# Kernel optimization log

Hardware: AMD Instinct MI355X
Metric: run time of the kernel (lower is better)

The kernel has to match this reference:

```python
import jax, jax.numpy as jnp
import numpy as np

N = 100000      # nodes
E = 1600000     # edges (before self loops)
F_IN = 256      # num_features
HID = 8         # hid per head, layer 1
H1 = 8          # in_head
H2 = 4          # out_head
NCLS = 40       # num_classes


def setup_inputs() -> dict:
    key = jax.random.key(0)
    ks = jax.random.split(key, 10)
    p = lambda k, shape: jax.random.normal(k, shape, jnp.float32) * 0.1
    d1 = H1 * HID   # 64
    d2 = H2 * NCLS  # 160
    return dict(
        x=jax.random.normal(ks[0], (N, F_IN), jnp.float32),
        edge_index=jax.random.randint(ks[1], (2, E), 0, N),
        Wl1=p(ks[2], (F_IN, d1)), bl1=jnp.zeros((d1,), jnp.float32),
        Wr1=p(ks[3], (F_IN, d1)), br1=jnp.zeros((d1,), jnp.float32),
        att1=p(ks[4], (H1, HID)), b1=jnp.zeros((d1,), jnp.float32),
        Wl2=p(ks[5], (d1, d2)), bl2=jnp.zeros((d2,), jnp.float32),
        Wr2=p(ks[6], (d1, d2)), br2=jnp.zeros((d2,), jnp.float32),
        att2=p(ks[7], (H2, NCLS)), b2=jnp.zeros((NCLS,), jnp.float32),
    )


def gatv2_conv(x, src, dst, Wl, bl, Wr, br, att, bias, heads, ch, concat):
    """PyG GATv2Conv (eval mode): lin_l -> source/messages, lin_r -> target."""
    n = x.shape[0]
    xl = (x @ Wl + bl).reshape(n, heads, ch)   # source-side features
    xr = (x @ Wr + br).reshape(n, heads, ch)   # target-side features
    # edge-wise attention logits: LeakyReLU(x_i + x_j) . att
    e = jax.nn.leaky_relu(xl[src] + xr[dst], 0.2)          # [E, H, C]
    logits = jnp.einsum('ehc,hc->eh', e, att)               # [E, H]
    # segment softmax over incoming edges of each destination node
    m = jax.ops.segment_max(logits, dst, num_segments=n)    # [N, H]
    ex = jnp.exp(logits - m[dst])
    s = jax.ops.segment_sum(ex, dst, num_segments=n)        # [N, H]
    alpha = ex / (s[dst] + 1e-16)                           # [E, H]
    # scatter-add weighted source messages
    out = jax.ops.segment_sum(xl[src] * alpha[:, :, None], dst, num_segments=n)  # [N, H, C]
    if concat:
        return out.reshape(n, heads * ch) + bias
    return out.mean(axis=1) + bias


def reference(x, edge_index, Wl1, bl1, Wr1, br1, att1, b1,
              Wl2, bl2, Wr2, br2, att2, b2):
    n = x.shape[0]
    loop = jnp.arange(n)
    # PyG GATv2Conv default add_self_loops=True
    src = jnp.concatenate([edge_index[0], loop])
    dst = jnp.concatenate([edge_index[1], loop])
    # eval mode: all dropout (input, inter-layer, attention) disabled
    h = gatv2_conv(x, src, dst, Wl1, bl1, Wr1, br1, att1, b1, H1, HID, True)
    h = jax.nn.elu(h)
    out = gatv2_conv(h, src, dst, Wl2, bl2, Wr2, br2, att2, b2, H2, NCLS, False)
    return jax.nn.log_softmax(out, axis=1)
```

## Files before the change

### kernel.cpp

```cpp
#include <hip/hip_runtime.h>
#include <math.h>

#define NN 100000
#define EE 1600000
#define FIN 256
#define D1 64
#define D2 160
#define C2 40
#define PK1 264
#define PK2 72
#define NBUCK 391
#define CAP 5000

typedef unsigned short u16;
typedef __attribute__((ext_vector_type(8))) short bf16x8;
typedef __attribute__((ext_vector_type(4))) float f32x4;

__device__ __forceinline__ float lrelu(float x){ return x > 0.f ? x : 0.2f*x; }
__device__ __forceinline__ float bf2f(u16 u){ return __uint_as_float((unsigned)u << 16); }
__device__ __forceinline__ u16 f2bf(float f){
  unsigned b = __float_as_uint(f);
  return (u16)((b + 0x7FFFu + ((b >> 16) & 1u)) >> 16);
}

__global__ __launch_bounds__(256) void part1_k(const int* __restrict__ ei,
                                               int* __restrict__ bcnt,
                                               int* __restrict__ csrtmp){
  __shared__ int hist[NBUCK];
  __shared__ int gbase[NBUCK];
  int t = threadIdx.x;
  for (int i = t; i < NBUCK; i += 256) hist[i] = 0;
  __syncthreads();
  int rb[8], rr[8], rv[8];
  #pragma unroll
  for (int q = 0; q < 8; ++q){
    int e = blockIdx.x*2048 + q*256 + t;
    rb[q] = -1;
    if (e < EE){
      int s = ei[e], d = ei[EE + e];
      int b = d >> 8;
      rb[q] = b;
      rv[q] = s | ((d & 255) << 17);
      rr[q] = atomicAdd(&hist[b], 1);
    }
  }
  __syncthreads();
  for (int i = t; i < NBUCK; i += 256)
    if (hist[i] > 0) gbase[i] = atomicAdd(&bcnt[i], hist[i]);
  __syncthreads();
  #pragma unroll
  for (int q = 0; q < 8; ++q){
    if (rb[q] >= 0){
      int pos = gbase[rb[q]] + rr[q];
      if (pos < CAP) csrtmp[rb[q]*CAP + pos] = rv[q];
    }
  }
}

__global__ __launch_bounds__(256) void sort_k(const int* __restrict__ bcnt,
                                              const int* __restrict__ csrtmp,
                                              int* __restrict__ csr,
                                              int* __restrict__ off,
                                              int* __restrict__ end){
  __shared__ int cnt[256];
  __shared__ int sc[256];
  __shared__ int cur[256];
  int b = blockIdx.x, t = threadIdx.x;
  int E = bcnt[b]; if (E > CAP) E = CAP;
  cnt[t] = 0;
  __syncthreads();
  for (int i = t; i < E; i += 256){
    int v = csrtmp[b*CAP + i];
    atomicAdd(&cnt[(v >> 17) & 255], 1);
  }
  __syncthreads();
  int x = cnt[t];
  sc[t] = x;
  __syncthreads();
  for (int o = 1; o < 256; o <<= 1){
    int v = (t >= o) ? sc[t - o] : 0;
    __syncthreads();
    sc[t] += v;
    __syncthreads();
  }
  int excl = sc[t] - x;
  cur[t] = excl;
  int n = (b << 8) + t;
  if (n < NN){
    off[n] = b*CAP + excl;
    end[n] = b*CAP + excl + x;
  }
  __syncthreads();
  for (int i = t; i < E; i += 256){
    int v = csrtmp[b*CAP + i];
    int p = atomicAdd(&cur[(v >> 17) & 255], 1);
    csr[b*CAP + p] = v & 0x1FFFF;
  }
}

__global__ __launch_bounds__(256) void gemm1_mfma(
    const float* __restrict__ X,
    const float* __restrict__ Wl, const float* __restrict__ bl,
    const float* __restrict__ Wr, const float* __restrict__ br,
    u16* __restrict__ outl, u16* __restrict__ outr){
  __shared__ u16 WB[128*PK1];
  int t = threadIdx.x;
  #pragma unroll
  for (int q = 0; q < 16; ++q){
    int idx = t + 256*q;
    int k = idx >> 4, c4 = idx & 15;
    float4 vl = *reinterpret_cast<const float4*>(Wl + (size_t)k*D1 + c4*4);
    float4 vr = *reinterpret_cast<const float4*>(Wr + (size_t)k*D1 + c4*4);
    WB[(c4*4+0)*PK1 + k] = f2bf(vl.x); WB[(c4*4+1)*PK1 + k] = f2bf(vl.y);
    WB[(c4*4+2)*PK1 + k] = f2bf(vl.z); WB[(c4*4+3)*PK1 + k] = f2bf(vl.w);
    WB[(64+c4*4+0)*PK1 + k] = f2bf(vr.x); WB[(64+c4*4+1)*PK1 + k] = f2bf(vr.y);
    WB[(64+c4*4+2)*PK1 + k] = f2bf(vr.z); WB[(64+c4*4+3)*PK1 + k] = f2bf(vr.w);
  }
  __syncthreads();
  int w = t >> 6, l = t & 63;
  int g = l >> 4;
  int arow = blockIdx.x*64 + w*16 + (l & 15);
  if (arow >= NN) arow = NN-1;
  const float* xp = X + (size_t)arow*FIN + g*8;
  f32x4 acc[8] = {};
  #pragma unroll
  for (int kk = 0; kk < 8; ++kk){
    float4 a0 = *reinterpret_cast<const float4*>(xp + kk*32);
    float4 a1 = *reinterpret_cast<const float4*>(xp + kk*32 + 4);
    union { bf16x8 v; u16 u[8]; } A;
    A.u[0]=f2bf(a0.x); A.u[1]=f2bf(a0.y); A.u[2]=f2bf(a0.z); A.u[3]=f2bf(a0.w);
    A.u[4]=f2bf(a1.x); A.u[5]=f2bf(a1.y); A.u[6]=f2bf(a1.z); A.u[7]=f2bf(a1.w);
    const u16* wb = WB + (l & 15)*PK1 + kk*32 + g*8;
    #pragma unroll
    for (int c = 0; c < 8; ++c){
      bf16x8 B = *reinterpret_cast<const bf16x8*>(wb + c*16*PK1);
      acc[c] = __builtin_amdgcn_mfma_f32_16x16x32_bf16(A.v, B, acc[c], 0, 0, 0);
    }
  }
  int ocol = l & 15;
  int orow0 = blockIdx.x*64 + w*16 + g*4;
  #pragma unroll
  for (int c = 0; c < 8; ++c){
    bool left = (c < 4);
    int col = (left ? c : c-4)*16 + ocol;
    u16* op = left ? outl : outr;
    float bv = (left ? bl : br)[col];
    #pragma unroll
    for (int r = 0; r < 4; ++r){
      int row = orow0 + r;
      if (row < NN) op[(size_t)row*D1 + col] = f2bf(acc[c][r] + bv);
    }
  }
}

__global__ __launch_bounds__(256) void gemm2_mfma(
    const u16* __restrict__ H,
    const float* __restrict__ Wl, const float* __restrict__ bl,
    const float* __restrict__ Wr, const float* __restrict__ br,
    u16* __restrict__ outl, u16* __restrict__ outr){
  __shared__ u16 WB[320*PK2];
  int t = threadIdx.x;
  #pragma unroll
  for (int q = 0; q < 10; ++q){
    int idx = t + 256*q;
    int k = idx / 40, c4 = idx % 40;
    float4 vl = *reinterpret_cast<const float4*>(Wl + (size_t)k*D2 + c4*4);
    float4 vr = *reinterpret_cast<const float4*>(Wr + (size_t)k*D2 + c4*4);
    WB[(c4*4+0)*PK2 + k] = f2bf(vl.x); WB[(c4*4+1)*PK2 + k] = f2bf(vl.y);
    WB[(c4*4+2)*PK2 + k] = f2bf(vl.z); WB[(c4*4+3)*PK2 + k] = f2bf(vl.w);
    WB[(160+c4*4+0)*PK2 + k] = f2bf(vr.x); WB[(160+c4*4+1)*PK2 + k] = f2bf(vr.y);
    WB[(160+c4*4+2)*PK2 + k] = f2bf(vr.z); WB[(160+c4*4+3)*PK2 + k] = f2bf(vr.w);
  }
  __syncthreads();
  int w = t >> 6, l = t & 63;
  int g = l >> 4;
  int arow = blockIdx.x*64 + w*16 + (l & 15);
  if (arow >= NN) arow = NN-1;
  const u16* hp = H + (size_t)arow*D1 + g*8;
  f32x4 acc[20] = {};
  #pragma unroll
  for (int kk = 0; kk < 2; ++kk){
    bf16x8 A = *reinterpret_cast<const bf16x8*>(hp + kk*32);
    const u16* wb = WB + (l & 15)*PK2 + kk*32 + g*8;
    #pragma unroll
    for (int c = 0; c < 20; ++c){
      bf16x8 B = *reinterpret_cast<const bf16x8*>(wb + c*16*PK2);
      acc[c] = __builtin_amdgcn_mfma_f32_16x16x32_bf16(A, B, acc[c], 0, 0, 0);
    }
  }
  int ocol = l & 15;
  int orow0 = blockIdx.x*64 + w*16 + g*4;
  #pragma unroll
  for (int c = 0; c < 20; ++c){
    bool left = (c < 10);
    int col = (left ? c : c-10)*16 + ocol;
    u16* op = left ? outl : outr;
    float bv = (left ? bl : br)[col];
    #pragma unroll
    for (int r = 0; r < 4; ++r){
      int row = orow0 + r;
      if (row < NN) op[(size_t)row*D2 + col] = f2bf(acc[c][r] + bv);
    }
  }
}

__global__ void l1_fused(const u16* __restrict__ xl, const u16* __restrict__ xr,
                         const int* __restrict__ off, const int* __restrict__ end,
                         const int* __restrict__ csr_src,
                         const float* __restrict__ att, const float* __restrict__ b,
                         u16* __restrict__ out){
  int n = blockIdx.x*4 + (threadIdx.x >> 6);
  if (n >= NN) return;
  int lane = threadIdx.x & 63;
  int g = lane >> 4, l = lane & 15;
  ushort4 xru = *reinterpret_cast<const ushort4*>(xr + (size_t)n*D1 + 4*l);
  float xrv[4] = {bf2f(xru.x), bf2f(xru.y), bf2f(xru.z), bf2f(xru.w)};
  float attv[4];
  #pragma unroll
  for (int k = 0; k < 4; ++k) attv[k] = att[4*l + k];
  ushort4 xsu = *reinterpret_cast<const ushort4*>(xl + (size_t)n*D1 + 4*l);
  float xsv[4] = {bf2f(xsu.x), bf2f(xsu.y), bf2f(xsu.z), bf2f(xsu.w)};
  float ts = 0.f;
  #pragma unroll
  for (int k = 0; k < 4; ++k) ts += lrelu(xsv[k] + xrv[k]) * attv[k];
  ts += __shfl_xor(ts, 1);
  float ps = (g == 0) ? __expf(ts) : 0.f;
  float s = ps, acc[4];
  #pragma unroll
  for (int k = 0; k < 4; ++k) acc[k] = ps * xsv[k];
  int e0 = off[n], e1 = end[n];
  int p = e0 + g;
  for (; p + 4 < e1; p += 8){
    int sa = csr_src[p], sb = csr_src[p+4];
    ushort4 ua = *reinterpret_cast<const ushort4*>(xl + (size_t)sa*D1 + 4*l);
    ushort4 ub = *reinterpret_cast<const ushort4*>(xl + (size_t)sb*D1 + 4*l);
    float xa[4] = {bf2f(ua.x), bf2f(ua.y), bf2f(ua.z), bf2f(ua.w)};
    float xb[4] = {bf2f(ub.x), bf2f(ub.y), bf2f(ub.z), bf2f(ub.w)};
    float ta = 0.f, tb = 0.f;
    #pragma unroll
    for (int k = 0; k < 4; ++k){
      ta += lrelu(xa[k] + xrv[k]) * attv[k];
      tb += lrelu(xb[k] + xrv[k]) * attv[k];
    }
    ta += __shfl_xor(ta, 1);
    tb += __shfl_xor(tb, 1);
    float pa = __expf(ta), pb = __expf(tb);
    s += pa + pb;
    #pragma unroll
    for (int k = 0; k < 4; ++k) acc[k] = fmaf(pa, xa[k], fmaf(pb, xb[k], acc[k]));
  }
  for (; p < e1; p += 4){
    int sa = csr_src[p];
    ushort4 ua = *reinterpret_cast<const ushort4*>(xl + (size_t)sa*D1 + 4*l);
    float xa[4] = {bf2f(ua.x), bf2f(ua.y), bf2f(ua.z), bf2f(ua.w)};
    float ta = 0.f;
    #pragma unroll
    for (int k = 0; k < 4; ++k) ta += lrelu(xa[k] + xrv[k]) * attv[k];
    ta += __shfl_xor(ta, 1);
    float pa = __expf(ta);
    s += pa;
    #pragma unroll
    for (int k = 0; k < 4; ++k) acc[k] = fmaf(pa, xa[k], acc[k]);
  }
  #pragma unroll
  for (int d = 16; d <= 32; d <<= 1){
    s += __shfl_xor(s, d);
    #pragma unroll
    for (int k = 0; k < 4; ++k) acc[k] += __shfl_xor(acc[k], d);
  }
  if (g == 0){
    float inv = 1.f / (s + 1e-16f);
    ushort4 o;
    float v0 = acc[0]*inv + b[4*l+0]; o.x = f2bf(v0 > 0.f ? v0 : expm1f(v0));
    float v1 = acc[1]*inv + b[4*l+1]; o.y = f2bf(v1 > 0.f ? v1 : expm1f(v1));
    float v2 = acc[2]*inv + b[4*l+2]; o.z = f2bf(v2 > 0.f ? v2 : expm1f(v2));
    float v3 = acc[3]*inv + b[4*l+3]; o.w = f2bf(v3 > 0.f ? v3 : expm1f(v3));
    *reinterpret_cast<ushort4*>(out + (size_t)n*D1 + 4*l) = o;
  }
}

__global__ void l2_fused(const u16* __restrict__ xl, const u16* __restrict__ xr,
                         const int* __restrict__ off, const int* __restrict__ end,
                         const int* __restrict__ csr_src,
                         const float* __restrict__ att, const float* __restrict__ b,
                         float* __restrict__ out){
  int n = blockIdx.x*4 + (threadIdx.x >> 6);
  if (n >= NN) return;
  int lane = threadIdx.x & 63;
  int g = lane >> 4, l = lane & 15;
  int c0 = 10*l;
  float xrv[10], attv[10];
  #pragma unroll
  for (int k2 = 0; k2 < 5; ++k2){
    ushort2 u = *reinterpret_cast<const ushort2*>(xr + (size_t)n*D2 + c0 + 2*k2);
    xrv[2*k2] = bf2f(u.x); xrv[2*k2+1] = bf2f(u.y);
  }
  #pragma unroll
  for (int k = 0; k < 10; ++k) attv[k] = att[c0 + k];
  float xsv[10];
  #pragma unroll
  for (int k2 = 0; k2 < 5; ++k2){
    ushort2 u = *reinterpret_cast<const ushort2*>(xl + (size_t)n*D2 + c0 + 2*k2);
    xsv[2*k2] = bf2f(u.x); xsv[2*k2+1] = bf2f(u.y);
  }
  float ts = 0.f;
  #pragma unroll
  for (int k = 0; k < 10; ++k) ts += lrelu(xsv[k] + xrv[k]) * attv[k];
  ts += __shfl_xor(ts, 1); ts += __shfl_xor(ts, 2);
  float ps = (g == 0) ? __expf(ts) : 0.f;
  float s = ps, acc[10];
  #pragma unroll
  for (int k = 0; k < 10; ++k) acc[k] = ps * xsv[k];
  int e0 = off[n], e1 = end[n];
  int p = e0 + g;
  for (; p + 4 < e1; p += 8){
    int sa = csr_src[p], sb = csr_src[p+4];
    float xa[10], xb[10];
    #pragma unroll
    for (int k2 = 0; k2 < 5; ++k2){
      ushort2 u = *reinterpret_cast<const ushort2*>(xl + (size_t)sa*D2 + c0 + 2*k2);
      xa[2*k2] = bf2f(u.x); xa[2*k2+1] = bf2f(u.y);
    }
    #pragma unroll
    for (int k2 = 0; k2 < 5; ++k2){
      ushort2 u = *reinterpret_cast<const ushort2*>(xl + (size_t)sb*D2 + c0 + 2*k2);
      xb[2*k2] = bf2f(u.x); xb[2*k2+1] = bf2f(u.y);
    }
    float ta = 0.f, tb = 0.f;
    #pragma unroll
    for (int k = 0; k < 10; ++k){
      ta += lrelu(xa[k] + xrv[k]) * attv[k];
      tb += lrelu(xb[k] + xrv[k]) * attv[k];
    }
    ta += __shfl_xor(ta, 1); ta += __shfl_xor(ta, 2);
    tb += __shfl_xor(tb, 1); tb += __shfl_xor(tb, 2);
    float pa = __expf(ta), pb = __expf(tb);
    s += pa + pb;
    #pragma unroll
    for (int k = 0; k < 10; ++k) acc[k] = fmaf(pa, xa[k], fmaf(pb, xb[k], acc[k]));
  }
  for (; p < e1; p += 4){
    int sa = csr_src[p];
    float xa[10];
    #pragma unroll
    for (int k2 = 0; k2 < 5; ++k2){
      ushort2 u = *reinterpret_cast<const ushort2*>(xl + (size_t)sa*D2 + c0 + 2*k2);
      xa[2*k2] = bf2f(u.x); xa[2*k2+1] = bf2f(u.y);
    }
    float ta = 0.f;
    #pragma unroll
    for (int k = 0; k < 10; ++k) ta += lrelu(xa[k] + xrv[k]) * attv[k];
    ta += __shfl_xor(ta, 1); ta += __shfl_xor(ta, 2);
    float pa = __expf(ta);
    s += pa;
    #pragma unroll
    for (int k = 0; k < 10; ++k) acc[k] = fmaf(pa, xa[k], acc[k]);
  }
  #pragma unroll
  for (int d = 16; d <= 32; d <<= 1){
    s += __shfl_xor(s, d);
    #pragma unroll
    for (int k = 0; k < 10; ++k) acc[k] += __shfl_xor(acc[k], d);
  }
  float inv = 1.f / (s + 1e-16f);
  float v[10];
  #pragma unroll
  for (int k = 0; k < 10; ++k){
    float o = acc[k] * inv;
    o += __shfl_xor(o, 4);
    o += __shfl_xor(o, 8);
    v[k] = o*0.25f + b[10*(l & 3) + k];
  }
  float mx = v[0];
  #pragma unroll
  for (int k = 1; k < 10; ++k) mx = fmaxf(mx, v[k]);
  mx = fmaxf(mx, __shfl_xor(mx, 1));
  mx = fmaxf(mx, __shfl_xor(mx, 2));
  float es = 0.f;
  #pragma unroll
  for (int k = 0; k < 10; ++k) es += __expf(v[k] - mx);
  es += __shfl_xor(es, 1);
  es += __shfl_xor(es, 2);
  float lse = mx + __logf(es);
  if (g == 0 && l < 4){
    float* op = out + (size_t)n*C2 + 10*l;
    #pragma unroll
    for (int k2 = 0; k2 < 5; ++k2)
      *reinterpret_cast<float2*>(op + 2*k2) = make_float2(v[2*k2] - lse, v[2*k2+1] - lse);
  }
}

extern "C" void kernel_launch(void* const* d_in, const int* in_sizes, int n_in,
                              void* d_out, int out_size, void* d_ws, size_t ws_size,
                              hipStream_t stream){
  const float* x    = (const float*)d_in[0];
  const int*   ei   = (const int*)  d_in[1];
  const float* Wl1  = (const float*)d_in[2];
  const float* bl1  = (const float*)d_in[3];
  const float* Wr1  = (const float*)d_in[4];
  const float* br1  = (const float*)d_in[5];
  const float* att1 = (const float*)d_in[6];
  const float* b1   = (const float*)d_in[7];
  const float* Wl2  = (const float*)d_in[8];
  const float* bl2  = (const float*)d_in[9];
  const float* Wr2  = (const float*)d_in[10];
  const float* br2  = (const float*)d_in[11];
  const float* att2 = (const float*)d_in[12];
  const float* b2   = (const float*)d_in[13];
  float* out = (float*)d_out;

  char* ws = (char*)d_ws;
  u16*   B1     = (u16*)(ws);
  u16*   B2     = (u16*)(ws + 13000000);
  u16*   h1     = (u16*)(ws + 26000000);
  u16*   B3     = (u16*)(ws + 39000000);
  u16*   B4     = (u16*)(ws + 72000000);
  int*   off    = (int*)(ws + 105000000);
  int*   end    = (int*)(ws + 106000000);
  int*   bcnt   = (int*)(ws + 107000000);
  int*   csrtmp = (int*)(ws + 108000000);
  int*   csr    = (int*)(ws + 116000000);
  const int blk = 256;
  const int MB = (NN + 63)/64;

  hipMemsetAsync(bcnt, 0, (size_t)NBUCK*4, stream);
  part1_k<<<(EE + 2047)/2048, blk, 0, stream>>>(ei, bcnt, csrtmp);
  sort_k <<<NBUCK, blk, 0, stream>>>(bcnt, csrtmp, csr, off, end);

  gemm1_mfma<<<MB, blk, 0, stream>>>(x, Wl1, bl1, Wr1, br1, B1, B2);
  l1_fused  <<<(NN + 3)/4, blk, 0, stream>>>(B1, B2, off, end, csr, att1, b1, h1);

  gemm2_mfma<<<MB, blk, 0, stream>>>(h1, Wl2, bl2, Wr2, br2, B3, B4);
  l2_fused  <<<(NN + 3)/4, blk, 0, stream>>>(B3, B4, off, end, csr, att2, b2, out);
}
```

Before: 364.2 us.

## Split LeakyReLU into linear plus abs term, precompute linear logits in GEMM

Rewrites the GATv2 score using leaky_relu(z) = 0.6z + 0.4|z|. The linear part becomes per-node dot products with att, folded into the weights (a new wprep kernel builds W·att) and produced as an extra MFMA output column in each GEMM. The edge loops then only evaluate the 0.4|xl+xr| term and add two per-node scalars loaded from a small fp32 array. The edge kernels also pack two nodes per wavefront, 2 edge groups each, instead of one node with 4 groups. This adds an extra gather per edge and a tiny single-block kernel, and it reorders the workspace so B4 and csrtmp now overlap.

```diff
diff --git a/kernel.cpp b/kernel.cpp
--- a/kernel.cpp
+++ b/kernel.cpp
@@ -16,11 +16,61 @@
 typedef __attribute__((ext_vector_type(8))) short bf16x8;
 typedef __attribute__((ext_vector_type(4))) float f32x4;
 
-__device__ __forceinline__ float lrelu(float x){ return x > 0.f ? x : 0.2f*x; }
 __device__ __forceinline__ float bf2f(u16 u){ return __uint_as_float((unsigned)u << 16); }
 __device__ __forceinline__ u16 f2bf(float f){
   unsigned b = __float_as_uint(f);
   return (u16)((b + 0x7FFFu + ((b >> 16) & 1u)) >> 16);
+}
+
+__global__ void wprep_k(const float* __restrict__ Wl1, const float* __restrict__ Wr1,
+                        const float* __restrict__ att1,
+                        const float* __restrict__ bl1, const float* __restrict__ br1,
+                        const float* __restrict__ Wl2, const float* __restrict__ Wr2,
+                        const float* __restrict__ att2,
+                        const float* __restrict__ bl2, const float* __restrict__ br2,
+                        float* __restrict__ WA1, float* __restrict__ BA1,
+                        float* __restrict__ WA2, float* __restrict__ BA2){
+  int t = threadIdx.x;
+  {
+    int k = t;
+    #pragma unroll
+    for (int j = 0; j < 16; ++j){
+      const float* W = (j < 8) ? Wl1 : Wr1;
+      int h = j & 7;
+      float s = 0.f;
+      #pragma unroll
+      for (int c = 0; c < 8; ++c) s += W[(size_t)k*D1 + h*8 + c] * att1[h*8 + c];
+      WA1[k*16 + j] = 0.6f * s;
+    }
+  }
+  if (t < 64){
+    int k = t;
+    #pragma unroll
+    for (int j = 0; j < 8; ++j){
+      const float* W = (j < 4) ? Wl2 : Wr2;
+      int h = j & 3;
+      float s = 0.f;
+      for (int c = 0; c < 40; ++c) s += W[(size_t)k*D2 + h*40 + c] * att2[h*40 + c];
+      WA2[k*8 + j] = 0.6f * s;
+    }
+  }
+  if (t >= 128 && t < 144){
+    int j = t - 128;
+    const float* B = (j < 8) ? bl1 : br1;
+    int h = j & 7;
+    float s = 0.f;
+    #pragma unroll
+    for (int c = 0; c < 8; ++c) s += B[h*8 + c] * att1[h*8 + c];
+    BA1[j] = 0.6f * s;
+  }
+  if (t >= 160 && t < 168){
+    int j = t - 160;
+    const float* B = (j < 4) ? bl2 : br2;
+    int h = j & 3;
+    float s = 0.f;
+    for (int c = 0; c < 40; ++c) s += B[h*40 + c] * att2[h*40 + c];
+    BA2[j] = 0.6f * s;
+  }
 }
 
 __global__ __launch_bounds__(256) void part1_k(const int* __restrict__ ei,
@@ -102,8 +152,9 @@
     const float* __restrict__ X,
     const float* __restrict__ Wl, const float* __restrict__ bl,
     const float* __restrict__ Wr, const float* __restrict__ br,
-    u16* __restrict__ outl, u16* __restrict__ outr){
-  __shared__ u16 WB[128*PK1];
+    const float* __restrict__ WA1, const float* __restrict__ BA1,
+    u16* __restrict__ outl, u16* __restrict__ outr, float* __restrict__ ALR){
+  __shared__ u16 WB[144*PK1];
   int t = threadIdx.x;
   #pragma unroll
   for (int q = 0; q < 16; ++q){
@@ -116,13 +167,19 @@
     WB[(64+c4*4+0)*PK1 + k] = f2bf(vr.x); WB[(64+c4*4+1)*PK1 + k] = f2bf(vr.y);
     WB[(64+c4*4+2)*PK1 + k] = f2bf(vr.z); WB[(64+c4*4+3)*PK1 + k] = f2bf(vr.w);
   }
+  #pragma unroll
+  for (int q = 0; q < 16; ++q){
+    int idx = t + 256*q;
+    int k = idx >> 4, j = idx & 15;
+    WB[(128+j)*PK1 + k] = f2bf(WA1[k*16 + j]);
+  }
   __syncthreads();
   int w = t >> 6, l = t & 63;
   int g = l >> 4;
   int arow = blockIdx.x*64 + w*16 + (l & 15);
   if (arow >= NN) arow = NN-1;
   const float* xp = X + (size_t)arow*FIN + g*8;
-  f32x4 acc[8] = {};
+  f32x4 acc[9] = {};
   #pragma unroll
   for (int kk = 0; kk < 8; ++kk){
     float4 a0 = *reinterpret_cast<const float4*>(xp + kk*32);
@@ -132,7 +189,7 @@
     A.u[4]=f2bf(a1.x); A.u[5]=f2bf(a1.y); A.u[6]=f2bf(a1.z); A.u[7]=f2bf(a1.w);
     const u16* wb = WB + (l & 15)*PK1 + kk*32 + g*8;
     #pragma unroll
-    for (int c = 0; c < 8; ++c){
+    for (int c = 0; c < 9; ++c){
       bf16x8 B = *reinterpret_cast<const bf16x8*>(wb + c*16*PK1);
       acc[c] = __builtin_amdgcn_mfma_f32_16x16x32_bf16(A.v, B, acc[c], 0, 0, 0);
     }
@@ -151,14 +208,23 @@
       if (row < NN) op[(size_t)row*D1 + col] = f2bf(acc[c][r] + bv);
     }
   }
+  {
+    float bav = BA1[ocol];
+    #pragma unroll
+    for (int r = 0; r < 4; ++r){
+      int row = orow0 + r;
+      if (row < NN) ALR[(size_t)row*16 + ocol] = acc[8][r] + bav;
+    }
+  }
 }
 
 __global__ __launch_bounds__(256) void gemm2_mfma(
     const u16* __restrict__ H,
     const float* __restrict__ Wl, const float* __restrict__ bl,
     const float* __restrict__ Wr, const float* __restrict__ br,
-    u16* __restrict__ outl, u16* __restrict__ outr){
-  __shared__ u16 WB[320*PK2];
+    const float* __restrict__ WA2, const float* __restrict__ BA2,
+    u16* __restrict__ outl, u16* __restrict__ outr, float* __restrict__ ALR){
+  __shared__ u16 WB[336*PK2];
   int t = threadIdx.x;
   #pragma unroll
   for (int q = 0; q < 10; ++q){
@@ -171,19 +237,26 @@
     WB[(160+c4*4+0)*PK2 + k] = f2bf(vr.x); WB[(160+c4*4+1)*PK2 + k] = f2bf(vr.y);
     WB[(160+c4*4+2)*PK2 + k] = f2bf(vr.z); WB[(160+c4*4+3)*PK2 + k] = f2bf(vr.w);
   }
+  #pragma unroll
+  for (int q = 0; q < 2; ++q){
+    int i2 = t + 256*q;
+    int k = i2 >> 3, j = i2 & 7;
+    WB[(320+j)*PK2 + k] = f2bf(WA2[k*8 + j]);
+    WB[(328+j)*PK2 + k] = 0;
+  }
   __syncthreads();
   int w = t >> 6, l = t & 63;
   int g = l >> 4;
   int arow = blockIdx.x*64 + w*16 + (l & 15);
   if (arow >= NN) arow = NN-1;
   const u16* hp = H + (size_t)arow*D1 + g*8;
-  f32x4 acc[20] = {};
+  f32x4 acc[21] = {};
   #pragma unroll
   for (int kk = 0; kk < 2; ++kk){
     bf16x8 A = *reinterpret_cast<const bf16x8*>(hp + kk*32);
     const u16* wb = WB + (l & 15)*PK2 + kk*32 + g*8;
     #pragma unroll
-    for (int c = 0; c < 20; ++c){
+    for (int c = 0; c < 21; ++c){
       bf16x8 B = *reinterpret_cast<const bf16x8*>(wb + c*16*PK2);
       acc[c] = __builtin_amdgcn_mfma_f32_16x16x32_bf16(A, B, acc[c], 0, 0, 0);
     }
@@ -202,72 +275,82 @@
       if (row < NN) op[(size_t)row*D2 + col] = f2bf(acc[c][r] + bv);
     }
   }
+  if (ocol < 8){
+    float bav = BA2[ocol];
+    #pragma unroll
+    for (int r = 0; r < 4; ++r){
+      int row = orow0 + r;
+      if (row < NN) ALR[(size_t)row*8 + ocol] = acc[20][r] + bav;
+    }
+  }
 }
 
 __global__ void l1_fused(const u16* __restrict__ xl, const u16* __restrict__ xr,
                          const int* __restrict__ off, const int* __restrict__ end,
-                         const int* __restrict__ csr_src,
-                         const float* __restrict__ att, const float* __restrict__ b,
-                         u16* __restrict__ out){
-  int n = blockIdx.x*4 + (threadIdx.x >> 6);
+                         const int* __restrict__ csr,
+                         const float* __restrict__ att, const float* __restrict__ ALR,
+                         const float* __restrict__ b, u16* __restrict__ out){
+  int tid = threadIdx.x;
+  int lane = tid & 63;
+  int nh = lane >> 5, g = (lane >> 4) & 1, l = lane & 15;
+  int n = blockIdx.x*8 + (tid >> 6)*2 + nh;
   if (n >= NN) return;
-  int lane = threadIdx.x & 63;
-  int g = lane >> 4, l = lane & 15;
+  int h = l >> 1;
   ushort4 xru = *reinterpret_cast<const ushort4*>(xr + (size_t)n*D1 + 4*l);
   float xrv[4] = {bf2f(xru.x), bf2f(xru.y), bf2f(xru.z), bf2f(xru.w)};
-  float attv[4];
-  #pragma unroll
-  for (int k = 0; k < 4; ++k) attv[k] = att[4*l + k];
+  float a04[4];
+  #pragma unroll
+  for (int k = 0; k < 4; ++k) a04[k] = 0.4f * att[4*l + k];
+  float ARn = ALR[(size_t)n*16 + 8 + h];
   ushort4 xsu = *reinterpret_cast<const ushort4*>(xl + (size_t)n*D1 + 4*l);
   float xsv[4] = {bf2f(xsu.x), bf2f(xsu.y), bf2f(xsu.z), bf2f(xsu.w)};
   float ts = 0.f;
   #pragma unroll
-  for (int k = 0; k < 4; ++k) ts += lrelu(xsv[k] + xrv[k]) * attv[k];
+  for (int k = 0; k < 4; ++k) ts += a04[k] * fabsf(xsv[k] + xrv[k]);
   ts += __shfl_xor(ts, 1);
-  float ps = (g == 0) ? __expf(ts) : 0.f;
+  float ps = (g == 0) ? __expf(ts + ALR[(size_t)n*16 + h] + ARn) : 0.f;
   float s = ps, acc[4];
   #pragma unroll
   for (int k = 0; k < 4; ++k) acc[k] = ps * xsv[k];
-  int e0 = off[n], e1 = end[n];
-  int p = e0 + g;
-  for (; p + 4 < e1; p += 8){
-    int sa = csr_src[p], sb = csr_src[p+4];
+  int p = off[n] + g, e1 = end[n];
+  for (; p + 2 < e1; p += 4){
+    int sa = csr[p], sb = csr[p+2];
     ushort4 ua = *reinterpret_cast<const ushort4*>(xl + (size_t)sa*D1 + 4*l);
     ushort4 ub = *reinterpret_cast<const ushort4*>(xl + (size_t)sb*D1 + 4*l);
+    float ALa = ALR[(size_t)sa*16 + h], ALb = ALR[(size_t)sb*16 + h];
     float xa[4] = {bf2f(ua.x), bf2f(ua.y), bf2f(ua.z), bf2f(ua.w)};
     float xb[4] = {bf2f(ub.x), bf2f(ub.y), bf2f(ub.z), bf2f(ub.w)};
     float ta = 0.f, tb = 0.f;
     #pragma unroll
     for (int k = 0; k < 4; ++k){
-      ta += lrelu(xa[k] + xrv[k]) * attv[k];
-      tb += lrelu(xb[k] + xrv[k]) * attv[k];
+      ta += a04[k] * fabsf(xa[k] + xrv[k]);
+      tb += a04[k] * fabsf(xb[k] + xrv[k]);
     }
     ta += __shfl_xor(ta, 1);
     tb += __shfl_xor(tb, 1);
-    float pa = __expf(ta), pb = __expf(tb);
+    float pa = __expf(ta + ALa + ARn);
+    float pb = __expf(tb + ALb + ARn);
     s += pa + pb;
     #pragma unroll
     for (int k = 0; k < 4; ++k) acc[k] = fmaf(pa, xa[k], fmaf(pb, xb[k], acc[k]));
   }
-  for (; p < e1; p += 4){
-    int sa = csr_src[p];
+  for (; p < e1; p += 2){
+    int sa = csr[p];
     ushort4 ua = *reinterpret_cast<const ushort4*>(xl + (size_t)sa*D1 + 4*l);
+    float ALa = ALR[(size_t)sa*16 + h];
     float xa[4] = {bf2f(ua.x), bf2f(ua.y), bf2f(ua.z), bf2f(ua.w)};
     float ta = 0.f;
     #pragma unroll
-    for (int k = 0; k < 4; ++k) ta += lrelu(xa[k] + xrv[k]) * attv[k];
+    for (int k = 0; k < 4; ++k) ta += a04[k] * fabsf(xa[k] + xrv[k]);
     ta += __shfl_xor(ta, 1);
-    float pa = __expf(ta);
+    float pa = __expf(ta + ALa + ARn);
     s += pa;
     #pragma unroll
     for (int k = 0; k < 4; ++k) acc[k] = fmaf(pa, xa[k], acc[k]);
   }
-  #pragma unroll
-  for (int d = 16; d <= 32; d <<= 1){
-    s += __shfl_xor(s, d);
-    #pragma unroll
-    for (int k = 0; k < 4; ++k) acc[k] += __shfl_xor(acc[k], d);
-  }
+  s += __shfl_xor(s, 16);
+  #pragma unroll
+  for (int k = 0; k < 4; ++k) acc[k] += __shfl_xor(acc[k], 16);
   if (g == 0){
     float inv = 1.f / (s + 1e-16f);
     ushort4 o;
@@ -281,22 +364,25 @@
 
 __global__ void l2_fused(const u16* __restrict__ xl, const u16* __restrict__ xr,
                          const int* __restrict__ off, const int* __restrict__ end,
-                         const int* __restrict__ csr_src,
-                         const float* __restrict__ att, const float* __restrict__ b,
-                         float* __restrict__ out){
-  int n = blockIdx.x*4 + (threadIdx.x >> 6);
+                         const int* __restrict__ csr,
+                         const float* __restrict__ att, const float* __restrict__ ALR,
+                         const float* __restrict__ b, float* __restrict__ out){
+  int tid = threadIdx.x;
+  int lane = tid & 63;
+  int nh = lane >> 5, g = (lane >> 4) & 1, l = lane & 15;
+  int n = blockIdx.x*8 + (tid >> 6)*2 + nh;
   if (n >= NN) return;
-  int lane = threadIdx.x & 63;
-  int g = lane >> 4, l = lane & 15;
+  int h = l >> 2;
   int c0 = 10*l;
-  float xrv[10], attv[10];
+  float xrv[10], a04[10];
   #pragma unroll
   for (int k2 = 0; k2 < 5; ++k2){
     ushort2 u = *reinterpret_cast<const ushort2*>(xr + (size_t)n*D2 + c0 + 2*k2);
     xrv[2*k2] = bf2f(u.x); xrv[2*k2+1] = bf2f(u.y);
   }
   #pragma unroll
-  for (int k = 0; k < 10; ++k) attv[k] = att[c0 + k];
+  for (int k = 0; k < 10; ++k) a04[k] = 0.4f * att[c0 + k];
+  float ARn = ALR[(size_t)n*8 + 4 + h];
   float xsv[10];
   #pragma unroll
   for (int k2 = 0; k2 < 5; ++k2){
@@ -305,16 +391,16 @@
   }
   float ts = 0.f;
   #pragma unroll
-  for (int k = 0; k < 10; ++k) ts += lrelu(xsv[k] + xrv[k]) * attv[k];
+  for (int k = 0; k < 10; ++k) ts += a04[k] * fabsf(xsv[k] + xrv[k]);
   ts += __shfl_xor(ts, 1); ts += __shfl_xor(ts, 2);
-  float ps = (g == 0) ? __expf(ts) : 0.f;
+  float ps = (g == 0) ? __expf(ts + ALR[(size_t)n*8 + h] + ARn) : 0.f;
   float s = ps, acc[10];
   #pragma unroll
   for (int k = 0; k < 10; ++k) acc[k] = ps * xsv[k];
-  int e0 = off[n], e1 = end[n];
-  int p = e0 + g;
-  for (; p + 4 < e1; p += 8){
-    int sa = csr_src[p], sb = csr_src[p+4];
+  int p = off[n] + g, e1 = end[n];
+  for (; p + 2 < e1; p += 4){
+    int sa = csr[p], sb = csr[p+2];
+    float ALa = ALR[(size_t)sa*8 + h], ALb = ALR[(size_t)sb*8 + h];
     float xa[10], xb[10];
     #pragma unroll
     for (int k2 = 0; k2 < 5; ++k2){
@@ -329,18 +415,20 @@
     float ta = 0.f, tb = 0.f;
     #pragma unroll
     for (int k = 0; k < 10; ++k){
-      ta += lrelu(xa[k] + xrv[k]) * attv[k];
-      tb += lrelu(xb[k] + xrv[k]) * attv[k];
+      ta += a04[k] * fabsf(xa[k] + xrv[k]);
+      tb += a04[k] * fabsf(xb[k] + xrv[k]);
     }
     ta += __shfl_xor(ta, 1); ta += __shfl_xor(ta, 2);
     tb += __shfl_xor(tb, 1); tb += __shfl_xor(tb, 2);
-    float pa = __expf(ta), pb = __expf(tb);
+    float pa = __expf(ta + ALa + ARn);
+    float pb = __expf(tb + ALb + ARn);
     s += pa + pb;
     #pragma unroll
     for (int k = 0; k < 10; ++k) acc[k] = fmaf(pa, xa[k], fmaf(pb, xb[k], acc[k]));
   }
-  for (; p < e1; p += 4){
-    int sa = csr_src[p];
+  for (; p < e1; p += 2){
+    int sa = csr[p];
+    float ALa = ALR[(size_t)sa*8 + h];
     float xa[10];
     #pragma unroll
     for (int k2 = 0; k2 < 5; ++k2){
@@ -349,19 +437,16 @@
     }
     float ta = 0.f;
     #pragma unroll
-    for (int k = 0; k < 10; ++k) ta += lrelu(xa[k] + xrv[k]) * attv[k];
+    for (int k = 0; k < 10; ++k) ta += a04[k] * fabsf(xa[k] + xrv[k]);
     ta += __shfl_xor(ta, 1); ta += __shfl_xor(ta, 2);
-    float pa = __expf(ta);
+    float pa = __expf(ta + ALa + ARn);
     s += pa;
     #pragma unroll
     for (int k = 0; k < 10; ++k) acc[k] = fmaf(pa, xa[k], acc[k]);
   }
-  #pragma unroll
-  for (int d = 16; d <= 32; d <<= 1){
-    s += __shfl_xor(s, d);
-    #pragma unroll
-    for (int k = 0; k < 10; ++k) acc[k] += __shfl_xor(acc[k], d);
-  }
+  s += __shfl_xor(s, 16);
+  #pragma unroll
+  for (int k = 0; k < 10; ++k) acc[k] += __shfl_xor(acc[k], 16);
   float inv = 1.f / (s + 1e-16f);
   float v[10];
   #pragma unroll
@@ -410,26 +495,34 @@
   float* out = (float*)d_out;
 
   char* ws = (char*)d_ws;
-  u16*   B1     = (u16*)(ws);
-  u16*   B2     = (u16*)(ws + 13000000);
-  u16*   h1     = (u16*)(ws + 26000000);
-  u16*   B3     = (u16*)(ws + 39000000);
-  u16*   B4     = (u16*)(ws + 72000000);
-  int*   off    = (int*)(ws + 105000000);
-  int*   end    = (int*)(ws + 106000000);
-  int*   bcnt   = (int*)(ws + 107000000);
-  int*   csrtmp = (int*)(ws + 108000000);
-  int*   csr    = (int*)(ws + 116000000);
+  u16*   B1     = (u16*)  (ws);
+  u16*   B2     = (u16*)  (ws + 13000000);
+  u16*   h1     = (u16*)  (ws + 26000000);
+  u16*   B3     = (u16*)  (ws + 39000000);
+  u16*   B4     = (u16*)  (ws + 71000000);
+  int*   csrtmp = (int*)  (ws + 71000000);
+  float* ALR1   = (float*)(ws + 103000000);
+  float* ALR2   = (float*)(ws + 110000000);
+  float* WA1    = (float*)(ws + 113300000);
+  float* BA1    = (float*)(ws + 113330000);
+  float* WA2    = (float*)(ws + 113340000);
+  float* BA2    = (float*)(ws + 113350000);
+  int*   off    = (int*)  (ws + 113400000);
+  int*   end    = (int*)  (ws + 113900000);
+  int*   bcnt   = (int*)  (ws + 114400000);
+  int*   csr    = (int*)  (ws + 114500000);
   const int blk = 256;
   const int MB = (NN + 63)/64;
 
   hipMemsetAsync(bcnt, 0, (size_t)NBUCK*4, stream);
   part1_k<<<(EE + 2047)/2048, blk, 0, stream>>>(ei, bcnt, csrtmp);
   sort_k <<<NBUCK, blk, 0, stream>>>(bcnt, csrtmp, csr, off, end);
-
-  gemm1_mfma<<<MB, blk, 0, stream>>>(x, Wl1, bl1, Wr1, br1, B1, B2);
-  l1_fused  <<<(NN + 3)/4, blk, 0, stream>>>(B1, B2, off, end, csr, att1, b1, h1);
-
-  gemm2_mfma<<<MB, blk, 0, stream>>>(h1, Wl2, bl2, Wr2, br2, B3, B4);
-  l2_fused  <<<(NN + 3)/4, blk, 0, stream>>>(B3, B4, off, end, csr, att2, b2, out);
-}
+  wprep_k<<<1, blk, 0, stream>>>(Wl1, Wr1, att1, bl1, br1,
+                                 Wl2, Wr2, att2, bl2, br2, WA1, BA1, WA2, BA2);
+
+  gemm1_mfma<<<MB, blk, 0, stream>>>(x, Wl1, bl1, Wr1, br1, WA1, BA1, B1, B2, ALR1);
+  l1_fused  <<<(NN + 7)/8, blk, 0, stream>>>(B1, B2, off, end, csr, att1, ALR1, b1, h1);
+
+  gemm2_mfma<<<MB, blk, 0, stream>>>(h1, Wl2, bl2, Wr2, br2, WA2, BA2, B3, B4, ALR2);
+  l2_fused  <<<(NN + 7)/8, blk, 0, stream>>>(B3, B4, off, end, csr, att2, ALR2, b2, out);
+}
```

Result: slower. 381.3 us (+4.7%).
